# Optimization experiments

Hardware: AMD Instinct MI355X
Metric: run time of the kernel (lower is better)

Reference implementation:

```python
import jax, jax.numpy as jnp
import numpy as np

D = 64      # latent dim (made.nin)
H = 512     # MADE hidden width

def _made_masks():
    # Standard MADE with sequential degrees (natural ordering).
    in_deg = np.arange(1, D + 1)                     # (D,)
    hid_deg = (np.arange(H) % (D - 1)) + 1           # (H,)
    out_deg = np.tile(in_deg, 2)                     # (2D,) mean+pre_scale share degrees
    M1 = (hid_deg[None, :] >= in_deg[:, None]).astype(np.float32)   # (D, H)
    M2 = (hid_deg[None, :] >= hid_deg[:, None]).astype(np.float32)  # (H, H)
    M3 = (out_deg[None, :] > hid_deg[:, None]).astype(np.float32)   # (H, 2D)
    return jnp.asarray(M1), jnp.asarray(M2), jnp.asarray(M3)

def setup_inputs() -> dict:
    key = jax.random.key(0)
    ks = jax.random.split(key, 8)
    B, S, C = 2048, 16, 256
    sc = 0.02
    return {
        'context': jax.random.normal(ks[0], (B, C), jnp.float32),
        'eps': jax.random.normal(ks[1], (S, B, D), jnp.float32),
        'W1': jax.random.normal(ks[2], (D, H), jnp.float32) * sc,
        'Wc': jax.random.normal(ks[3], (C, H), jnp.float32) * sc,
        'b1': jnp.zeros((H,), jnp.float32),
        'W2': jax.random.normal(ks[4], (H, H), jnp.float32) * sc,
        'b2': jnp.zeros((H,), jnp.float32),
        'W3': jax.random.normal(ks[5], (H, 2 * D), jnp.float32) * sc,
        'b3': jnp.zeros((2 * D,), jnp.float32),
    }

def reference(context, eps, W1, Wc, b1, W2, b2, W3, b3):
    M1, M2, M3 = _made_masks()
    S, B, _ = eps.shape
    ctx_proj = context @ Wc + b1                 # (B, H), constant across steps
    MW1, MW2, MW3 = M1 * W1, M2 * W2, M3 * W3

    def step(z, d):
        # z: (S, B, D) current partial sample
        h1 = jax.nn.relu(z @ MW1 + ctx_proj[None])          # (S, B, H)
        h2 = jax.nn.relu(h1 @ MW2 + b2)                     # (S, B, H)
        out = h2 @ MW3 + b3                                 # (S, B, 2D)
        mu, pre_scale = out[..., :D], out[..., D:]
        scale = jax.nn.softplus(pre_scale)
        onehot = jax.nn.one_hot(d, D, dtype=z.dtype)        # (D,)
        mu_d = (mu * onehot).sum(-1)                        # (S, B)
        scale_d = (scale * onehot).sum(-1)                  # (S, B)
        eps_d = (eps * onehot).sum(-1)                      # (S, B)
        z_d = mu_d + scale_d * eps_d                        # reparameterized Normal sample
        z = z + z_d[..., None] * onehot
        return z, (mu_d, scale_d)

    z0 = jnp.zeros((S, B, D), eps.dtype)
    z_samples, (mus, scales) = jax.lax.scan(step, z0, jnp.arange(D))
    mus = jnp.moveaxis(mus, 0, -1)       # (S, B, D)
    scales = jnp.moveaxis(scales, 0, -1) # (S, B, D)
    return z_samples, mus, scales
```

## Files before the change

### kernel.cpp

```cpp
#include <hip/hip_runtime.h>
#include <hip/hip_bf16.h>

#define ROWS 32
#define TPB 512

typedef unsigned short u16;
typedef __attribute__((ext_vector_type(8))) short bf16x8;
typedef __attribute__((ext_vector_type(16))) float f32x16;

__device__ __forceinline__ int deg_of_sorted(int i) {
  return (i < 72) ? (i / 9 + 1) : ((i - 8) / 8 + 1);
}
__device__ __forceinline__ int perm_of_sorted(int i) {
  int g, k;
  if (i < 72) { g = i / 9 + 1; k = i % 9; }
  else        { g = (i - 8) / 8 + 1; k = (i - 8) % 8; }
  return (g - 1) + 63 * k;
}
__device__ __forceinline__ int cum_deg(int d) {
  return (d <= 0) ? 0 : ((d <= 8) ? 9 * d : 8 * d + 8);
}
__device__ __forceinline__ u16 f2bfu(float x) {
  return __builtin_bit_cast(u16, __float2bfloat16(x));
}
__device__ __forceinline__ float softplus_f(float x) {
  return fmaxf(x, 0.f) + __logf(1.f + __expf(-fabsf(x)));
}

__global__ __launch_bounds__(256) void prep_w(
    const float* __restrict__ W1, const float* __restrict__ W2,
    const float* __restrict__ b2, const float* __restrict__ W3,
    float* __restrict__ mw1s, u16* __restrict__ mw2f,
    float* __restrict__ mw3f, float* __restrict__ b2s) {
  int idx = blockIdx.x * 256 + threadIdx.x;
  if (idx < 262144) {
    int kb = idx >> 12, n = (idx >> 3) & 511, kk = idx & 7;
    int k = kb * 8 + kk;
    float v = (deg_of_sorted(k) <= deg_of_sorted(n))
                  ? W2[perm_of_sorted(k) * 512 + perm_of_sorted(n)] : 0.f;
    mw2f[idx] = f2bfu(v);
    return;
  }
  idx -= 262144;
  if (idx < 32768) {
    int d = idx >> 9, j = idx & 511;
    mw1s[idx] = (deg_of_sorted(j) >= d + 1) ? W1[d * 512 + perm_of_sorted(j)] : 0.f;
    return;
  }
  idx -= 32768;
  if (idx < 65536) {
    int c = idx >> 9, j = idx & 511;
    mw3f[idx] = (deg_of_sorted(j) <= (c & 63)) ? W3[perm_of_sorted(j) * 128 + c] : 0.f;
    return;
  }
  idx -= 65536;
  if (idx < 512) b2s[idx] = b2[perm_of_sorted(idx)];
}

__global__ __launch_bounds__(512) void prep_ctx(
    const float* __restrict__ context, const float* __restrict__ Wc,
    const float* __restrict__ b1, float* __restrict__ ctxp) {
  __shared__ float cs[16][257];
  const int tid = threadIdx.x;
  const int b0  = blockIdx.x * 16;
  for (int i = tid; i < 16 * 256; i += 512) {
    int r = i >> 8, c = i & 255;
    cs[r][c] = context[(b0 + r) * 256 + c];
  }
  __syncthreads();
  const int j  = tid;
  const int pj = perm_of_sorted(j);
  float acc[16];
  const float bv = b1[pj];
  #pragma unroll
  for (int r = 0; r < 16; ++r) acc[r] = bv;
  for (int c = 0; c < 256; c += 4) {
    float w0 = Wc[(c + 0) * 512 + pj];
    float w1 = Wc[(c + 1) * 512 + pj];
    float w2 = Wc[(c + 2) * 512 + pj];
    float w3 = Wc[(c + 3) * 512 + pj];
    #pragma unroll
    for (int r = 0; r < 16; ++r) {
      acc[r] += cs[r][c + 0] * w0 + cs[r][c + 1] * w1 +
                cs[r][c + 2] * w2 + cs[r][c + 3] * w3;
    }
  }
  #pragma unroll
  for (int r = 0; r < 16; ++r) ctxp[(b0 + r) * 512 + j] = acc[r];
}

__global__ __launch_bounds__(TPB, 4) void made_main(
    const float* __restrict__ eps, const float* __restrict__ b3,
    const float* __restrict__ ctxp, const float* __restrict__ mw1s,
    const float* __restrict__ mw3f, const float* __restrict__ b2sg,
    const u16* __restrict__ mw2f, float* __restrict__ out) {
  __shared__ __align__(16) u16   dbuf[2][32][40];
  __shared__ __align__(16) float part2mu[9 * 33];
  __shared__ __align__(16) float part2sc[9 * 33];
  __shared__ __align__(16) float w1s[512];
  __shared__ __align__(16) float w3fs[2][2][512];
  __shared__ __align__(16) float b3s[128];
  __shared__ __align__(16) float epsall[ROWS * 65];
  __shared__ __align__(16) float zLb[ROWS * 65];
  __shared__ __align__(16) float muLb[ROWS * 65];
  __shared__ __align__(16) float scLb[ROWS * 65];

  const int tid  = threadIdx.x;
  const int lane = tid & 63;
  const int wave = tid >> 6;
  const int g0   = blockIdx.x * ROWS;
  const int b0   = g0 & 2047;

  const int rA = tid & 31;
  const int jA = (tid >> 5) << 5;
  float a1r[32];
  #pragma unroll
  for (int t = 0; t < 8; ++t) {
    *(float4*)&a1r[t * 4] = *(const float4*)&ctxp[(b0 + rA) * 512 + jA + t * 4];
  }

  ((unsigned*)dbuf)[tid] = 0u;
  ((unsigned*)dbuf)[tid + 512] = 0u;
  if (tid < 256) ((unsigned*)dbuf)[tid + 1024] = 0u;
  if (tid < 128) b3s[tid] = b3[tid];
  {
    int r = tid >> 4, c = (tid & 15) * 4;
    float4 ev = *(const float4*)&eps[(g0 + r) * 64 + c];
    epsall[r * 65 + c + 0] = ev.x;
    epsall[r * 65 + c + 1] = ev.y;
    epsall[r * 65 + c + 2] = ev.z;
    epsall[r * 65 + c + 3] = ev.w;
  }
  if (tid < 256) {
    int c_sel = tid >> 7, j0 = (tid & 127) * 4;
    *(float4*)&w3fs[0][c_sel][j0] = *(const float4*)&mw3f[(c_sel * 64) * 512 + j0];
  }
  __syncthreads();

  const int m  = lane & 31;
  const int kq = lane >> 5;
  const int jt0 = wave;
  const int jt1 = 15 - wave;
  const u16* bLane = mw2f + ((kq * 512 + m) << 3);
  const u16* bp0   = bLane + jt0 * 256;
  const u16* bp1   = bLane + jt1 * 256;
  const int ke0full = cum_deg(deg_of_sorted(jt0 * 32 + 31));
  const int ke1full = cum_deg(deg_of_sorted(jt1 * 32 + 31));

  f32x16 acc0, acc1;
  #pragma unroll
  for (int i = 0; i < 16; ++i) {
    const int ni = (i & 3) + 8 * (i >> 2) + 4 * kq;
    acc0[i] = b2sg[jt0 * 32 + ni];
    acc1[i] = b2sg[jt1 * 32 + ni];
  }

  for (int d = 0; d < 64; ++d) {
    const int Cd    = cum_deg(d);
    const int Cnext = cum_deg(d + 1);
    const int Cprev = cum_deg(d - 1);
    const int cb    = d & 1;
    const int nb    = cb ^ 1;

    float4 w1stg;
    if (tid < 128) w1stg = *(const float4*)&mw1s[d * 512 + tid * 4];
    float4 w3stg;
    int c_sel = 0, j0 = 0;
    if (tid >= 128 && tid < 384 && d < 63) {
      int t2 = tid - 128;
      c_sel = t2 >> 7; j0 = (t2 & 127) * 4;
      w3stg = *(const float4*)&mw3f[(c_sel * 64 + d + 1) * 512 + j0];
    }

    if (d > 0) {
      const int kb  = Cprev >> 4;
      const int nks = ((Cd - 1) >> 4) - kb + 1;
      #pragma unroll 2
      for (int t = 0; t < nks; ++t) {
        const int ks = kb + t;
        bf16x8 dF = *(const bf16x8*)&dbuf[cb][m][t * 16 + kq * 8];
        if (ke0full > ks * 16) {
          bf16x8 wA = *(const bf16x8*)(bp0 + ks * 8192);
          acc0 = __builtin_amdgcn_mfma_f32_32x32x16_bf16(wA, dF, acc0, 0, 0, 0);
        }
        if (ke1full > ks * 16) {
          bf16x8 wB = *(const bf16x8*)(bp1 + ks * 8192);
          acc1 = __builtin_amdgcn_mfma_f32_32x32x16_bf16(wB, dF, acc1, 0, 0, 0);
        }
      }
    }

    {
      const float* w3c = &w3fs[cb][0][0];
      float pmu = 0.f, psc = 0.f;
      if (jt0 * 32 < Cd) {
        #pragma unroll
        for (int g = 0; g < 4; ++g) {
          const int n0 = jt0 * 32 + 8 * g + 4 * kq;
          const float4 m0 = *(const float4*)&w3c[n0];
          const float4 s0 = *(const float4*)&w3c[512 + n0];
          float h0 = fmaxf(acc0[4 * g + 0], 0.f);
          float h1 = fmaxf(acc0[4 * g + 1], 0.f);
          float h2 = fmaxf(acc0[4 * g + 2], 0.f);
          float h3 = fmaxf(acc0[4 * g + 3], 0.f);
          pmu += h0 * m0.x + h1 * m0.y + h2 * m0.z + h3 * m0.w;
          psc += h0 * s0.x + h1 * s0.y + h2 * s0.z + h3 * s0.w;
        }
      }
      if (jt1 * 32 < Cd) {
        #pragma unroll
        for (int g = 0; g < 4; ++g) {
          const int n1 = jt1 * 32 + 8 * g + 4 * kq;
          const float4 m1 = *(const float4*)&w3c[n1];
          const float4 s1 = *(const float4*)&w3c[512 + n1];
          float h0 = fmaxf(acc1[4 * g + 0], 0.f);
          float h1 = fmaxf(acc1[4 * g + 1], 0.f);
          float h2 = fmaxf(acc1[4 * g + 2], 0.f);
          float h3 = fmaxf(acc1[4 * g + 3], 0.f);
          pmu += h0 * m1.x + h1 * m1.y + h2 * m1.z + h3 * m1.w;
          psc += h0 * s1.x + h1 * s1.y + h2 * s1.z + h3 * s1.w;
        }
      }
      pmu += __shfl_xor(pmu, 32);
      psc += __shfl_xor(psc, 32);
      if (kq == 0) part2mu[wave * 33 + m] = pmu;
      else         part2sc[wave * 33 + m] = psc;
    }

    ((unsigned*)dbuf[nb])[tid] = 0u;
    if (tid < 128) ((unsigned*)dbuf[nb])[512 + tid] = 0u;

    if (tid < 128) *(float4*)&w1s[tid * 4] = w1stg;
    else if (tid < 384 && d < 63) *(float4*)&w3fs[nb][c_sel][j0] = w3stg;
    __syncthreads();

    float msum = b3s[d], ssum = b3s[64 + d];
    #pragma unroll
    for (int w = 0; w < 8; ++w) {
      msum += part2mu[w * 33 + rA];
      ssum += part2sc[w * 33 + rA];
    }
    const float mu = msum;
    const float sc = softplus_f(ssum);
    const float z  = fmaf(sc, epsall[rA * 65 + d], mu);
    if (tid < 32) {
      zLb[rA * 65 + d]  = z;
      muLb[rA * 65 + d] = mu;
      scLb[rA * 65 + d] = sc;
    }

    const int kbw = Cd >> 4;
    if (jA >= Cd) {
      #pragma unroll
      for (int i = 0; i < 32; ++i) a1r[i] += z * w1s[jA + i];
    } else if (jA + 31 >= Cd) {
      #pragma unroll
      for (int i = 0; i < 32; ++i) {
        int j = jA + i;
        if (j >= Cd) a1r[i] += z * w1s[j];
      }
    }
    if (jA < Cnext && jA + 31 >= Cd) {
      #pragma unroll
      for (int i = 0; i < 32; ++i) {
        int j = jA + i;
        if (j >= Cd && j < Cnext) {
          dbuf[nb][rA][j - kbw * 16] = f2bfu(fmaxf(a1r[i], 0.f));
        }
      }
    }
    __syncthreads();
  }

  {
    const int r = tid >> 4, c = (tid & 15) * 4;
    float4 zv, mv, sv;
    zv.x = zLb[r * 65 + c + 0]; zv.y = zLb[r * 65 + c + 1];
    zv.z = zLb[r * 65 + c + 2]; zv.w = zLb[r * 65 + c + 3];
    mv.x = muLb[r * 65 + c + 0]; mv.y = muLb[r * 65 + c + 1];
    mv.z = muLb[r * 65 + c + 2]; mv.w = muLb[r * 65 + c + 3];
    sv.x = scLb[r * 65 + c + 0]; sv.y = scLb[r * 65 + c + 1];
    sv.z = scLb[r * 65 + c + 2]; sv.w = scLb[r * 65 + c + 3];
    *(float4*)&out[(g0 + r) * 64 + c]           = zv;
    *(float4*)&out[2097152 + (g0 + r) * 64 + c] = mv;
    *(float4*)&out[4194304 + (g0 + r) * 64 + c] = sv;
  }
}

extern "C" void kernel_launch(void* const* d_in, const int* in_sizes, int n_in,
                              void* d_out, int out_size, void* d_ws, size_t ws_size,
                              hipStream_t stream) {
  (void)in_sizes; (void)n_in; (void)out_size; (void)ws_size;
  const float* context = (const float*)d_in[0];
  const float* eps     = (const float*)d_in[1];
  const float* W1      = (const float*)d_in[2];
  const float* Wc      = (const float*)d_in[3];
  const float* b1      = (const float*)d_in[4];
  const float* W2      = (const float*)d_in[5];
  const float* b2      = (const float*)d_in[6];
  const float* W3      = (const float*)d_in[7];
  const float* b3      = (const float*)d_in[8];
  float* out = (float*)d_out;

  float* ws   = (float*)d_ws;
  float* ctxp = ws;
  float* mw1s = ctxp + 1048576;
  float* b2s  = mw1s + 32768;
  float* mw3f = b2s + 512;
  u16*   mw2f = (u16*)(mw3f + 65536);

  prep_w<<<1410, 256, 0, stream>>>(W1, W2, b2, W3, mw1s, mw2f, mw3f, b2s);
  prep_ctx<<<128, 512, 0, stream>>>(context, Wc, b1, ctxp);
  made_main<<<1024, TPB, 0, stream>>>(eps, b3, ctxp, mw1s, mw3f, b2s, mw2f, out);
}
```

Before: 622.0 us.

## Prefetch W2 MFMA fragments one step ahead and double-buffer W1 rows

Replaces the variable-length guarded W2 MFMA loop with a fixed two-k-step pair of MFMAs per tile. The W2 fragments for those two k-steps are loaded from global memory one iteration ahead into registers, so the load latency overlaps the rest of the step. W1 rows are now double-buffered in shared memory with the next row prefetched, like W3 already was. The cross-half shuffle reduction of mu/scale partials is replaced by 16 per-half slots summed by each half, plus one shuffle to exchange mu and scale. This removes load latency and branching from the serial 64-step critical path. In exchange it always issues four MFMAs per step, some on masked-zero weights, and adds register pressure.

```diff
diff --git a/kernel.cpp b/kernel.cpp
--- a/kernel.cpp
+++ b/kernel.cpp
@@ -95,9 +95,9 @@
     const float* __restrict__ mw3f, const float* __restrict__ b2sg,
     const u16* __restrict__ mw2f, float* __restrict__ out) {
   __shared__ __align__(16) u16   dbuf[2][32][40];
-  __shared__ __align__(16) float part2mu[9 * 33];
-  __shared__ __align__(16) float part2sc[9 * 33];
-  __shared__ __align__(16) float w1s[512];
+  __shared__ __align__(16) float part2mu[16 * 33];
+  __shared__ __align__(16) float part2sc[16 * 33];
+  __shared__ __align__(16) float w1fs[2][512];
   __shared__ __align__(16) float w3fs[2][2][512];
   __shared__ __align__(16) float b3s[128];
   __shared__ __align__(16) float epsall[ROWS * 65];
@@ -122,7 +122,10 @@
   ((unsigned*)dbuf)[tid] = 0u;
   ((unsigned*)dbuf)[tid + 512] = 0u;
   if (tid < 256) ((unsigned*)dbuf)[tid + 1024] = 0u;
-  if (tid < 128) b3s[tid] = b3[tid];
+  if (tid < 128) {
+    b3s[tid] = b3[tid];
+    *(float4*)&w1fs[0][tid * 4] = *(const float4*)&mw1s[tid * 4];
+  }
   {
     int r = tid >> 4, c = (tid & 15) * 4;
     float4 ev = *(const float4*)&eps[(g0 + r) * 64 + c];
@@ -144,8 +147,6 @@
   const u16* bLane = mw2f + ((kq * 512 + m) << 3);
   const u16* bp0   = bLane + jt0 * 256;
   const u16* bp1   = bLane + jt1 * 256;
-  const int ke0full = cum_deg(deg_of_sorted(jt0 * 32 + 31));
-  const int ke1full = cum_deg(deg_of_sorted(jt1 * 32 + 31));
 
   f32x16 acc0, acc1;
   #pragma unroll
@@ -155,39 +156,41 @@
     acc1[i] = b2sg[jt1 * 32 + ni];
   }
 
+  bf16x8 pfA0 = {}, pfA1 = {}, pfB0 = {}, pfB1 = {};
+
   for (int d = 0; d < 64; ++d) {
     const int Cd    = cum_deg(d);
     const int Cnext = cum_deg(d + 1);
-    const int Cprev = cum_deg(d - 1);
     const int cb    = d & 1;
     const int nb    = cb ^ 1;
 
-    float4 w1stg;
-    if (tid < 128) w1stg = *(const float4*)&mw1s[d * 512 + tid * 4];
-    float4 w3stg;
+    float4 w1stg, w3stg;
     int c_sel = 0, j0 = 0;
-    if (tid >= 128 && tid < 384 && d < 63) {
-      int t2 = tid - 128;
-      c_sel = t2 >> 7; j0 = (t2 & 127) * 4;
-      w3stg = *(const float4*)&mw3f[(c_sel * 64 + d + 1) * 512 + j0];
+    if (d < 63) {
+      if (tid < 128) w1stg = *(const float4*)&mw1s[(d + 1) * 512 + tid * 4];
+      else if (tid < 384) {
+        int t2 = tid - 128;
+        c_sel = t2 >> 7; j0 = (t2 & 127) * 4;
+        w3stg = *(const float4*)&mw3f[(c_sel * 64 + d + 1) * 512 + j0];
+      }
     }
 
     if (d > 0) {
-      const int kb  = Cprev >> 4;
-      const int nks = ((Cd - 1) >> 4) - kb + 1;
-      #pragma unroll 2
-      for (int t = 0; t < nks; ++t) {
-        const int ks = kb + t;
-        bf16x8 dF = *(const bf16x8*)&dbuf[cb][m][t * 16 + kq * 8];
-        if (ke0full > ks * 16) {
-          bf16x8 wA = *(const bf16x8*)(bp0 + ks * 8192);
-          acc0 = __builtin_amdgcn_mfma_f32_32x32x16_bf16(wA, dF, acc0, 0, 0, 0);
-        }
-        if (ke1full > ks * 16) {
-          bf16x8 wB = *(const bf16x8*)(bp1 + ks * 8192);
-          acc1 = __builtin_amdgcn_mfma_f32_32x32x16_bf16(wB, dF, acc1, 0, 0, 0);
-        }
-      }
+      bf16x8 dF0 = *(const bf16x8*)&dbuf[cb][m][kq * 8];
+      bf16x8 dF1 = *(const bf16x8*)&dbuf[cb][m][16 + kq * 8];
+      acc0 = __builtin_amdgcn_mfma_f32_32x32x16_bf16(pfA0, dF0, acc0, 0, 0, 0);
+      acc1 = __builtin_amdgcn_mfma_f32_32x32x16_bf16(pfB0, dF0, acc1, 0, 0, 0);
+      acc0 = __builtin_amdgcn_mfma_f32_32x32x16_bf16(pfA1, dF1, acc0, 0, 0, 0);
+      acc1 = __builtin_amdgcn_mfma_f32_32x32x16_bf16(pfB1, dF1, acc1, 0, 0, 0);
+    }
+
+    {
+      const int kbn  = (Cd >> 4) > 31 ? 31 : (Cd >> 4);
+      const int kbn1 = kbn + 1 > 31 ? 31 : kbn + 1;
+      pfA0 = *(const bf16x8*)(bp0 + kbn * 8192);
+      pfA1 = *(const bf16x8*)(bp0 + kbn1 * 8192);
+      pfB0 = *(const bf16x8*)(bp1 + kbn * 8192);
+      pfB1 = *(const bf16x8*)(bp1 + kbn1 * 8192);
     }
 
     {
@@ -221,43 +224,46 @@
           psc += h0 * s1.x + h1 * s1.y + h2 * s1.z + h3 * s1.w;
         }
       }
-      pmu += __shfl_xor(pmu, 32);
-      psc += __shfl_xor(psc, 32);
-      if (kq == 0) part2mu[wave * 33 + m] = pmu;
-      else         part2sc[wave * 33 + m] = psc;
+      const int slot = (wave * 2 + kq) * 33 + m;
+      part2mu[slot] = pmu;
+      part2sc[slot] = psc;
     }
 
     ((unsigned*)dbuf[nb])[tid] = 0u;
     if (tid < 128) ((unsigned*)dbuf[nb])[512 + tid] = 0u;
 
-    if (tid < 128) *(float4*)&w1s[tid * 4] = w1stg;
-    else if (tid < 384 && d < 63) *(float4*)&w3fs[nb][c_sel][j0] = w3stg;
+    if (d < 63) {
+      if (tid < 128) *(float4*)&w1fs[nb][tid * 4] = w1stg;
+      else if (tid < 384) *(float4*)&w3fs[nb][c_sel][j0] = w3stg;
+    }
     __syncthreads();
 
-    float msum = b3s[d], ssum = b3s[64 + d];
-    #pragma unroll
-    for (int w = 0; w < 8; ++w) {
-      msum += part2mu[w * 33 + rA];
-      ssum += part2sc[w * 33 + rA];
-    }
-    const float mu = msum;
-    const float sc = softplus_f(ssum);
-    const float z  = fmaf(sc, epsall[rA * 65 + d], mu);
-    if (tid < 32) {
-      zLb[rA * 65 + d]  = z;
-      muLb[rA * 65 + d] = mu;
-      scLb[rA * 65 + d] = sc;
+    float z, mu, sc;
+    {
+      const float* pb = kq ? &part2sc[0] : &part2mu[0];
+      float own = kq ? b3s[64 + d] : b3s[d];
+      #pragma unroll
+      for (int s = 0; s < 16; ++s) own += pb[s * 33 + m];
+      float other = __shfl_xor(own, 32);
+      mu = kq ? other : own;
+      sc = softplus_f(kq ? own : other);
+      z  = fmaf(sc, epsall[m * 65 + d], mu);
+      if (tid < 32) {
+        zLb[m * 65 + d]  = z;
+        muLb[m * 65 + d] = mu;
+        scLb[m * 65 + d] = sc;
+      }
     }
 
     const int kbw = Cd >> 4;
     if (jA >= Cd) {
       #pragma unroll
-      for (int i = 0; i < 32; ++i) a1r[i] += z * w1s[jA + i];
+      for (int i = 0; i < 32; ++i) a1r[i] += z * w1fs[cb][jA + i];
     } else if (jA + 31 >= Cd) {
       #pragma unroll
       for (int i = 0; i < 32; ++i) {
         int j = jA + i;
-        if (j >= Cd) a1r[i] += z * w1s[j];
+        if (j >= Cd) a1r[i] += z * w1fs[cb][j];
       }
     }
     if (jA < Cnext && jA + 31 >= Cd) {
```

After: 820.0 us. 31.8% more time.
